# Kernel tuning notes

Hardware: AMD Instinct MI355X
Metric: run time of the kernel (lower is better)

Reference implementation:

```python
import jax, jax.numpy as jnp
from jax import lax
import numpy as np

K = 2000      # self.k: entries kept per sample
T_SC = 3      # number of IHT iterations
DN = ('NCHW', 'OIHW', 'NCHW')


def keep_k_largest(X, k):
    # Per-sample hard threshold: keep the k largest-magnitude entries of the
    # flattened [C,H,W] activations, zero the rest (exactly k kept, as in argsort).
    B = X.shape[0]
    flat = X.reshape(B, -1)                                # [B, N]
    _, idx = lax.top_k(jnp.abs(flat), k)                   # [B, k]
    vals = jnp.take_along_axis(flat, idx, axis=1)          # [B, k]
    out = jnp.zeros_like(flat).at[jnp.arange(B)[:, None], idx].set(vals)
    return out.reshape(X.shape)


def _D_apply(X, W_D):
    # ConvTranspose2d(numb_atom -> dp_channels), stride 1, no padding:
    # full correlation with the spatially flipped, io-swapped kernel.
    kh, kw = W_D.shape[2], W_D.shape[3]
    Wt = jnp.flip(jnp.transpose(W_D, (1, 0, 2, 3)), (2, 3))  # [dp, atoms, kh, kw]
    return lax.conv_general_dilated(X, Wt, (1, 1),
                                    [(kh - 1, kh - 1), (kw - 1, kw - 1)],
                                    dimension_numbers=DN)


def _Dt_apply(Z, W_D):
    # Conv2d(dp_channels -> numb_atom) VALID; D_trans.weight = D.weight.permute(0,1,3,2)
    Wt = jnp.transpose(W_D, (0, 1, 3, 2))                  # [atoms, dp, kh, kw]
    return lax.conv_general_dilated(Z, Wt, (1, 1), 'VALID', dimension_numbers=DN)


def setup_inputs() -> dict:
    key = jax.random.key(0)
    k1, k2, k3 = jax.random.split(key, 3)
    Y = jax.random.normal(k1, (32, 3, 64, 64), jnp.float32)
    X0 = jax.random.normal(k2, (32, 128, 57, 57), jnp.float32)   # random init X in forward
    W_D = jax.random.normal(k3, (128, 3, 8, 8), jnp.float32) * 0.05
    return {"Y": Y, "X0": X0, "W_D": W_D}


def reference(Y, X0, W_D):
    # HT_arg = X - D_trans(D(X) - Y); then T_SC hard-threshold iterations.
    HT_arg = X0 - _Dt_apply(_D_apply(X0, W_D) - Y, W_D)
    X = HT_arg
    for i in range(T_SC):
        X = keep_k_largest(HT_arg, K)
        if i < T_SC - 1:  # final HT_arg update in the original is unused
            HT_arg = X - _Dt_apply(_D_apply(X, W_D) - Y, W_D)
    return X
```

## Files before the change

kernel.cpp:

```cpp
#include <hip/hip_runtime.h>

#define BATCH 32
#define ATOMS 128
#define CCH 3
#define XH 57
#define XW 57
#define OHH 64
#define OWW 64
#define KSEL 2000
#define PIX (XH*XW)
#define NPS (ATOMS*PIX)
#define NTOT (BATCH*NPS)
#define RPS (CCH*OHH*OWW)
#define RTOT (BATCH*RPS)
#define CANDCAP 32768
#define NW 24576
#define WSEG 102

__global__ __launch_bounds__(256) void prep_k(const float* __restrict__ Wg,
    double* __restrict__ WDd, double* __restrict__ Wt2d,
    const float* __restrict__ Y, double* __restrict__ Rd) {
  int e = blockIdx.x * 256 + threadIdx.x;
  if (e < NW) {
    {
      int kw = e & 7; int t = e >> 3; int c = t % 3; t /= 3; int kh = t & 7; int a = t >> 3;
      WDd[e] = (double)Wg[(a*3 + c)*64 + kh*8 + kw];
    }
    {
      int a = e & 127; int t = e >> 7; int j = t & 7; int i = (t >> 3) & 7; int c = t >> 6;
      Wt2d[e] = (double)Wg[(a*3 + c)*64 + j*8 + i];
    }
  }
  if (e < RTOT) Rd[e] = -(double)Y[e];
}

__global__ __launch_bounds__(256) void convD_k(const float* __restrict__ X,
    const double* __restrict__ WDd, double* __restrict__ Rd) {
  __shared__ float Xs[8][11][72];
  int p = blockIdx.x;
  int lg = (p & 7) * 256 + (p >> 3);
  int b = lg >> 6; int rem = lg & 63;
  int band = rem >> 2, quarter = rem & 3;
  int row0 = band * 4;
  int a_base = quarter * 32;
  int tid = threadIdx.x;
  int ox = tid & 63;
  int wv = __builtin_amdgcn_readfirstlane(tid >> 6);
  const float* Xb = X + (size_t)b * NPS;

  double acc[4][3];
#pragma unroll
  for (int ty = 0; ty < 4; ++ty)
#pragma unroll
    for (int c = 0; c < 3; ++c) acc[ty][c] = 0.0;

  for (int ch = 0; ch < 4; ++ch) {
    __syncthreads();
    for (int e = tid; e < 8 * 11 * 72; e += 256) {
      int ai = e / 792; int rem2 = e - ai * 792;
      int r = rem2 / 72; int ss = rem2 - r * 72;
      int gy = row0 - 7 + r;
      int xcol = ss - 7;
      int a = a_base + ch * 8 + ai;
      float v = 0.0f;
      if ((unsigned)xcol < (unsigned)XW && (unsigned)gy < (unsigned)XH)
        v = Xb[a * PIX + gy * XW + xcol];
      Xs[ai][r][ss] = v;
    }
    __syncthreads();
#pragma unroll
    for (int jj = 0; jj < 2; ++jj) {
      int ai = (wv << 1) + jj;
      int a  = a_base + ch * 8 + ai;
      const double* Wa = WDd + a * 192;
#pragma unroll
      for (int r = 0; r < 11; ++r) {
        int gy = row0 - 7 + r;
        if ((unsigned)gy >= (unsigned)XH) continue;
        double xd[8];
#pragma unroll
        for (int t = 0; t < 8; ++t) xd[t] = (double)Xs[ai][r][ox + t];
#pragma unroll
        for (int ty = 0; ty < 4; ++ty) {
          int kh = ty + 7 - r;
          if ((unsigned)kh < 8u) {
            const double* Wk = Wa + kh * 24;
#pragma unroll
            for (int kw = 0; kw < 8; ++kw) {
              acc[ty][0] = fma(xd[7 - kw], Wk[kw],      acc[ty][0]);
              acc[ty][1] = fma(xd[7 - kw], Wk[8 + kw],  acc[ty][1]);
              acc[ty][2] = fma(xd[7 - kw], Wk[16 + kw], acc[ty][2]);
            }
          }
        }
      }
    }
  }
#pragma unroll
  for (int ty = 0; ty < 4; ++ty) {
    int oy = row0 + ty;
#pragma unroll
    for (int c = 0; c < 3; ++c)
      atomicAdd(&Rd[((size_t)(b * CCH + c) << 12) + (oy << 6) + ox], acc[ty][c]);
  }
}

__global__ __launch_bounds__(256) void convD_sparse_k(const float* __restrict__ Wg,
    const int* __restrict__ nzidx, const float* __restrict__ nzval,
    const float* __restrict__ Y, float* __restrict__ R) {
  __shared__ double accd[512];
  __shared__ float Wf[8192];
  __shared__ int   li[KSEL];
  __shared__ float lv[KSEL];
  int p = blockIdx.x;
  int lg = (p & 7) * 96 + (p >> 3);
  int s = lg / 24; int r = lg % 24; int c = r >> 3; int band = r & 7;
  int row0 = band * 8;
  int tid = threadIdx.x;
  for (int e = tid; e < 512; e += 256) accd[e] = 0.0;
  for (int e = tid; e < 8192; e += 256) {
    int a = e >> 6, k2 = e & 63;
    Wf[e] = Wg[(a * 3 + c) * 64 + k2];
  }
  for (int e = tid; e < KSEL; e += 256) {
    li[e] = nzidx[s * KSEL + e];
    lv[e] = nzval[s * KSEL + e];
  }
  __syncthreads();
  int slot = tid >> 3, kw = tid & 7;
  for (int e = slot; e < KSEL; e += 32) {
    int idx = li[e];
    int a = (int)((unsigned)idx / 3249u);
    int pp = idx - a * 3249;
    int y = (int)((unsigned)pp / 57u);
    int x = pp - y * 57;
    int dy = y - row0;
    if (dy < -7 || dy > 7) continue;
    double val = (double)lv[e];
    const float* wp = Wf + (a << 6) + kw;
#pragma unroll
    for (int kh = 0; kh < 8; ++kh) {
      int rr = dy + kh;
      if ((unsigned)rr < 8u)
        __hip_atomic_fetch_add(&accd[(rr << 6) + x + kw],
                               val * (double)wp[kh << 3],
                               __ATOMIC_RELAXED, __HIP_MEMORY_SCOPE_WORKGROUP);
    }
  }
  __syncthreads();
  const float* Yb = Y + (((size_t)(s * CCH + c)) << 12) + (row0 << 6);
  float* Rb = R + (((size_t)(s * CCH + c)) << 12) + (row0 << 6);
  for (int e = tid; e < 512; e += 256)
    Rb[e] = (float)(accd[e] - (double)Yb[e]);
}

template <typename TR>
__global__ __launch_bounds__(256) void convDt_k(const TR* __restrict__ R,
    const double* __restrict__ Wt2d, const float* __restrict__ Xprev,
    float* __restrict__ HT, unsigned* __restrict__ g1) {
  __shared__ float Rl[3][15][72];
  __shared__ unsigned hh[1024];
  int p = blockIdx.x;
  int lg = (p & 7) * 512 + (p >> 3);
  int b = lg >> 7; int rem = lg & 127; int ag = rem >> 3; int by = rem & 7;
  int row0 = by * 8;
  int a0 = ag * 8;
  int tid = threadIdx.x;
  for (int e = tid; e < 1024; e += 256) hh[e] = 0;
  for (int e = tid; e < 3 * 15 * 72; e += 256) {
    int c = e / (15 * 72); int r2 = e - c * (15 * 72);
    int rr = r2 / 72; int cc = r2 - rr * 72;
    int gr = row0 + rr;
    float v = 0.0f;
    if (cc < OWW && gr < OHH)
      v = (float)R[((size_t)(b * CCH + c) << 12) + (gr << 6) + cc];
    Rl[c][rr][cc] = v;
  }
  __syncthreads();
  int x = tid & 63, yg = tid >> 6;
  int yb = yg * 2;
  double acc[8][2];
#pragma unroll
  for (int aa = 0; aa < 8; ++aa) { acc[aa][0] = 0.0; acc[aa][1] = 0.0; }

#pragma unroll 1
  for (int c = 0; c < 3; ++c) {
#pragma unroll 1
    for (int j = 0; j < 8; ++j) {
      double rw[9];
#pragma unroll
      for (int r = 0; r < 9; ++r) rw[r] = (double)Rl[c][yb + r][x + j];
#pragma unroll
      for (int i = 0; i < 8; ++i) {
        const double* wp = Wt2d + ((c * 8 + i) * 8 + j) * 128 + a0;
#pragma unroll
        for (int aa = 0; aa < 8; ++aa) {
          double w = wp[aa];
          acc[aa][0] = fma(rw[i + 0], w, acc[aa][0]);
          acc[aa][1] = fma(rw[i + 1], w, acc[aa][1]);
        }
      }
    }
  }
  if (x < XW) {
#pragma unroll
    for (int ty = 0; ty < 2; ++ty) {
      int yy = row0 + yb + ty;
      if (yy < XH) {
#pragma unroll
        for (int aa = 0; aa < 8; ++aa) {
          size_t xo = (size_t)(b * ATOMS + a0 + aa) * PIX + yy * XW + x;
          float fv = (float)((double)Xprev[xo] - acc[aa][ty]);
          HT[xo] = fv;
          unsigned u = __float_as_uint(fv) & 0x7fffffffu;
          unsigned bin = u >> 20;
          atomicAdd(&hh[bin >> 1], 1u << ((bin & 1) << 4));
        }
      }
    }
  }
  __syncthreads();
  unsigned* gp = g1 + (size_t)b * 2048;
  for (int e = tid; e < 1024; e += 256) {
    unsigned v = hh[e];
    unsigned lo = v & 0xffffu, hi = v >> 16;
    if (lo) atomicAdd(&gp[2 * e], lo);
    if (hi) atomicAdd(&gp[2 * e + 1], hi);
  }
}

template <int NB>
__global__ __launch_bounds__(256) void find_k(const unsigned* __restrict__ gh,
    const int* __restrict__ Kin, int* __restrict__ Bout, int* __restrict__ Kout) {
  int s = blockIdx.x;
  const unsigned* h = gh + s * NB;
  __shared__ unsigned part[256];
  constexpr int C = NB / 256;
  int t = threadIdx.x;
  unsigned sum = 0;
#pragma unroll
  for (int e = 0; e < C; ++e) sum += h[t * C + e];
  part[t] = sum;
  __syncthreads();
  if (t == 0) {
    int Kv = Kin ? Kin[s] : KSEL;
    unsigned cumBefore = 0;
    int bsel = 0;
    for (int q = 255; q >= 0; --q) {
      unsigned ps = part[q];
      if ((int)(cumBefore + ps) >= Kv) {
        for (int e = q * C + C - 1;; --e) {
          unsigned c2 = cumBefore + h[e];
          if ((int)c2 >= Kv) { bsel = e; break; }
          cumBefore = c2;
        }
        break;
      }
      cumBefore += ps;
    }
    Bout[s] = bsel;
    Kout[s] = Kv - (int)cumBefore;
  }
}

__global__ __launch_bounds__(256) void hist2_k(const float* __restrict__ HT,
    const int* __restrict__ b1, unsigned* __restrict__ g2,
    int* __restrict__ cand, int* __restrict__ candcnt) {
  __shared__ unsigned h[1024];
  __shared__ int lidx[4096];
  __shared__ int lcnt, lbase;
  for (int e = threadIdx.x; e < 1024; e += 256) h[e] = 0;
  if (threadIdx.x == 0) lcnt = 0;
  __syncthreads();
  int s = blockIdx.x >> 5;
  int chunk = blockIdx.x & 31;
  unsigned pre = (unsigned)b1[s];
  const uint4* U4 = (const uint4*)(HT + (size_t)s * NPS);
  for (int i4 = chunk * 256 + threadIdx.x; i4 < NPS / 4; i4 += 32 * 256) {
    uint4 v = U4[i4];
    unsigned uu[4] = {v.x, v.y, v.z, v.w};
#pragma unroll
    for (int t = 0; t < 4; ++t) {
      unsigned u = uu[t] & 0x7fffffffu;
      if ((u >> 20) == pre) {
        atomicAdd(&h[(u >> 10) & 1023], 1u);
        int pos = atomicAdd(&lcnt, 1);
        if (pos < 4096) lidx[pos] = i4 * 4 + t;
      }
    }
  }
  __syncthreads();
  if (threadIdx.x == 0) {
    int n = lcnt < 4096 ? lcnt : 4096;
    lbase = atomicAdd(&candcnt[s], n);
  }
  __syncthreads();
  int n = lcnt < 4096 ? lcnt : 4096;
  int base = lbase;
  for (int e = threadIdx.x; e < n; e += 256) {
    int g = base + e;
    if (g < CANDCAP) cand[s * CANDCAP + g] = lidx[e];
  }
  for (int e = threadIdx.x; e < 1024; e += 256)
    if (h[e]) atomicAdd(&g2[s * 1024 + e], h[e]);
}

__global__ __launch_bounds__(256) void pass3_k(const float* __restrict__ HT,
    const int* __restrict__ cand, const int* __restrict__ candcnt,
    const int* __restrict__ b1, const unsigned* __restrict__ g2,
    const int* __restrict__ k1, unsigned* __restrict__ tau_out,
    int* __restrict__ cutoff_out) {
  int s = blockIdx.x;
  __shared__ unsigned h[1024];
  __shared__ unsigned part[256];
  __shared__ int eqidx[1024];
  __shared__ int eqn;
  __shared__ unsigned tau_sh;
  __shared__ int k3_sh;
  __shared__ int b2_sh, k2_sh;
  int t = threadIdx.x;
  const unsigned* hg = g2 + s * 1024;
  unsigned sum = 0;
#pragma unroll
  for (int e = 0; e < 4; ++e) sum += hg[t * 4 + e];
  part[t] = sum;
  for (int e = t; e < 1024; e += 256) h[e] = 0;
  if (t == 0) eqn = 0;
  __syncthreads();
  if (t == 0) {
    int Kv = k1[s];
    unsigned cumBefore = 0;
    int bsel = 0;
    for (int q = 255; q >= 0; --q) {
      unsigned ps = part[q];
      if ((int)(cumBefore + ps) >= Kv) {
        for (int e = q * 4 + 3;; --e) {
          unsigned c2 = cumBefore + hg[e];
          if ((int)c2 >= Kv) { bsel = e; break; }
          cumBefore = c2;
        }
        break;
      }
      cumBefore += ps;
    }
    b2_sh = bsel;
    k2_sh = Kv - (int)cumBefore;
  }
  __syncthreads();
  int n = candcnt[s];
  if (n > CANDCAP) n = CANDCAP;
  unsigned pre21 = (((unsigned)b1[s]) << 10) | (unsigned)b2_sh;
  const unsigned* U = (const unsigned*)(HT + (size_t)s * NPS);
  for (int e = t; e < n; e += 256) {
    int i = cand[s * CANDCAP + e];
    unsigned u = U[i] & 0x7fffffffu;
    if ((u >> 10) == pre21) atomicAdd(&h[u & 1023], 1u);
  }
  __syncthreads();
  if (t == 0) {
    int Kv = k2_sh;
    unsigned cumBefore = 0;
    int b3 = 0;
    for (int e = 1023; e >= 0; --e) {
      unsigned c2 = cumBefore + h[e];
      if ((int)c2 >= Kv) { b3 = e; break; }
      cumBefore = c2;
    }
    tau_sh = (pre21 << 10) | (unsigned)b3;
    k3_sh = Kv - (int)cumBefore;
  }
  __syncthreads();
  unsigned tau = tau_sh;
  for (int e = t; e < n; e += 256) {
    int i = cand[s * CANDCAP + e];
    unsigned u = U[i] & 0x7fffffffu;
    if (u == tau) {
      int pos = atomicAdd(&eqn, 1);
      if (pos < 1024) eqidx[pos] = i;
    }
  }
  __syncthreads();
  if (t == 0) {
    int m = eqn < 1024 ? eqn : 1024;
    int k3 = k3_sh;
    int cutoff;
    if (k3 >= m) {
      cutoff = 0x7fffffff;
    } else {
      int last = -1;
      for (int r = 0; r < k3; ++r) {
        int mn = 0x7fffffff;
        for (int q = 0; q < m; ++q) {
          int v = eqidx[q];
          if (v > last && v < mn) mn = v;
        }
        last = mn;
      }
      cutoff = last;
    }
    tau_out[s] = tau;
    cutoff_out[s] = cutoff;
  }
}

__global__ __launch_bounds__(256) void write_k(const float* __restrict__ HT,
    const unsigned* __restrict__ tau, const int* __restrict__ cutoff,
    float* __restrict__ Xo, int* __restrict__ nzidx, float* __restrict__ nzval,
    int* __restrict__ nzcnt) {
  __shared__ int lidx[2048];
  __shared__ float lval[2048];
  __shared__ int lcnt, lbase;
  int s = blockIdx.x / WSEG;
  int seg = blockIdx.x % WSEG;
  int tid = threadIdx.x;
  bool emit = (nzidx != nullptr);
  if (tid == 0) lcnt = 0;
  __syncthreads();
  unsigned tt = tau[s];
  int co = cutoff[s];
  size_t sbase = (size_t)s * NPS;
  const float4* H4 = (const float4*)(HT + sbase);
  float4* X4 = (float4*)(Xo + sbase);
  int f0 = seg * 1024;
#pragma unroll
  for (int rr = 0; rr < 4; ++rr) {
    int i4 = f0 + rr * 256 + tid;
    if (i4 < NPS / 4) {
      float4 v = H4[i4];
      float vv[4] = {v.x, v.y, v.z, v.w};
      float oo[4];
#pragma unroll
      for (int t = 0; t < 4; ++t) {
        int il = i4 * 4 + t;
        unsigned u = __float_as_uint(vv[t]) & 0x7fffffffu;
        bool keep = (u > tt) || (u == tt && il <= co);
        oo[t] = keep ? vv[t] : 0.0f;
        if (keep && emit) {
          int pos = atomicAdd(&lcnt, 1);
          if (pos < 2048) { lidx[pos] = il; lval[pos] = vv[t]; }
        }
      }
      X4[i4] = make_float4(oo[0], oo[1], oo[2], oo[3]);
    }
  }
  if (!emit) return;
  __syncthreads();
  if (tid == 0) lbase = atomicAdd(&nzcnt[s], lcnt);
  __syncthreads();
  int n = lcnt < 2048 ? lcnt : 2048;
  int base = lbase;
  for (int e = tid; e < n; e += 256) {
    int g = base + e;
    if (g < KSEL) { nzidx[s * KSEL + g] = lidx[e]; nzval[s * KSEL + g] = lval[e]; }
  }
}

extern "C" void kernel_launch(void* const* d_in, const int* in_sizes, int n_in,
                              void* d_out, int out_size, void* d_ws, size_t ws_size,
                              hipStream_t stream) {
  const float* Y  = (const float*)d_in[0];
  const float* X0 = (const float*)d_in[1];
  const float* Wg = (const float*)d_in[2];
  float* Xout = (float*)d_out;

  double* WDd  = (double*)d_ws;
  double* Wt2d = WDd + NW;
  float* HT   = (float*)(Wt2d + NW);
  float* Rbuf = HT + NTOT;
  double* Rd  = (double*)(Rbuf + RTOT);
  unsigned* g1 = (unsigned*)(Rd + RTOT);
  unsigned* g2 = g1 + 32 * 2048;
  int* candcnt = (int*)(g2 + 32 * 1024);
  int* nzcnt = candcnt + 32;
  int* b1 = nzcnt + 32;
  int* k1 = b1 + 32;
  unsigned* tau = (unsigned*)(k1 + 32);
  int* cutoff = (int*)(tau + 32);
  int* cand = cutoff + 32;
  int* nzidx = cand + 32 * CANDCAP;
  float* nzval = (float*)(nzidx + 32 * KSEL);
  size_t zero_bytes = (size_t)(32 * 2048 + 32 * 1024 + 32 + 32) * 4;

  prep_k<<<dim3((RTOT + 255) / 256), dim3(256), 0, stream>>>(Wg, WDd, Wt2d, Y, Rd);

  for (int it = 0; it < 3; ++it) {
    const float* Xsrc = (it == 0) ? X0 : (const float*)Xout;
    hipMemsetAsync(g1, 0, zero_bytes, stream);
    if (it == 0) {
      convD_k<<<dim3(2048), dim3(256), 0, stream>>>(Xsrc, WDd, Rd);
      convDt_k<double><<<dim3(4096), dim3(256), 0, stream>>>(Rd, Wt2d, Xsrc, HT, g1);
    } else {
      convD_sparse_k<<<dim3(BATCH * CCH * 8), dim3(256), 0, stream>>>(
          Wg, nzidx, nzval, Y, Rbuf);
      convDt_k<float><<<dim3(4096), dim3(256), 0, stream>>>(Rbuf, Wt2d, Xsrc, HT, g1);
    }
    find_k<2048><<<dim3(BATCH), dim3(256), 0, stream>>>(g1, (const int*)nullptr, b1, k1);
    hist2_k<<<dim3(BATCH * 32), dim3(256), 0, stream>>>(HT, b1, g2, cand, candcnt);
    pass3_k<<<dim3(BATCH), dim3(256), 0, stream>>>(HT, cand, candcnt, b1, g2, k1, tau, cutoff);
    bool last = (it == 2);
    write_k<<<dim3(BATCH * WSEG), dim3(256), 0, stream>>>(HT, tau, cutoff, Xout,
        last ? nullptr : nzidx, last ? nullptr : nzval, nzcnt);
  }
}
```

Measured before the change: 1.006 ms.

## Rebuild sparse X in shared memory and drop dense X writes until last iteration

In iterations after the first, convDt now scatters the sparse nonzero list (nzidx/nzval) into a shared-memory tile instead of reading the dense previous X from global memory. Because of that, write_k only stores the dense thresholded X on the final iteration. The separate find_k launch is removed, and the first-level histogram bin selection is recomputed redundantly inside hist2_k and pass3_k. Together these cut large dense global reads and writes plus one launch per iteration, at the cost of extra shared memory, a scan over 2000 nonzeros per block, and duplicated prefix-scan work.

```diff
diff --git a/kernel.cpp b/kernel.cpp
--- a/kernel.cpp
+++ b/kernel.cpp
@@ -154,12 +154,14 @@
     Rb[e] = (float)(accd[e] - (double)Yb[e]);
 }
 
-template <typename TR>
+template <typename TR, bool SPX>
 __global__ __launch_bounds__(256) void convDt_k(const TR* __restrict__ R,
     const double* __restrict__ Wt2d, const float* __restrict__ Xprev,
+    const int* __restrict__ nzidx, const float* __restrict__ nzval,
     float* __restrict__ HT, unsigned* __restrict__ g1) {
   __shared__ float Rl[3][15][72];
   __shared__ unsigned hh[1024];
+  __shared__ float Xp[8][8][XW];
   int p = blockIdx.x;
   int lg = (p & 7) * 512 + (p >> 3);
   int b = lg >> 7; int rem = lg & 127; int ag = rem >> 3; int by = rem & 7;
@@ -176,6 +178,19 @@
       v = (float)R[((size_t)(b * CCH + c) << 12) + (gr << 6) + cc];
     Rl[c][rr][cc] = v;
   }
+  if constexpr (SPX) {
+    for (int e = tid; e < 8 * 8 * XW; e += 256) (&Xp[0][0][0])[e] = 0.0f;
+    __syncthreads();
+    for (int e = tid; e < KSEL; e += 256) {
+      int idx = nzidx[b * KSEL + e];
+      int a = (int)((unsigned)idx / 3249u);
+      int pp2 = idx - a * 3249;
+      int yy = (int)((unsigned)pp2 / 57u);
+      int xx = pp2 - yy * 57;
+      if ((unsigned)(a - a0) < 8u && (unsigned)(yy - row0) < 8u)
+        Xp[a - a0][yy - row0][xx] = nzval[b * KSEL + e];
+    }
+  }
   __syncthreads();
   int x = tid & 63, yg = tid >> 6;
   int yb = yg * 2;
@@ -210,7 +225,10 @@
 #pragma unroll
         for (int aa = 0; aa < 8; ++aa) {
           size_t xo = (size_t)(b * ATOMS + a0 + aa) * PIX + yy * XW + x;
-          float fv = (float)((double)Xprev[xo] - acc[aa][ty]);
+          double xprev;
+          if constexpr (SPX) xprev = (double)Xp[aa][yb + ty][x];
+          else               xprev = (double)Xprev[xo];
+          float fv = (float)(xprev - acc[aa][ty]);
           HT[xo] = fv;
           unsigned u = __float_as_uint(fv) & 0x7fffffffu;
           unsigned bin = u >> 20;
@@ -229,28 +247,33 @@
   }
 }
 
-template <int NB>
-__global__ __launch_bounds__(256) void find_k(const unsigned* __restrict__ gh,
-    const int* __restrict__ Kin, int* __restrict__ Bout, int* __restrict__ Kout) {
-  int s = blockIdx.x;
-  const unsigned* h = gh + s * NB;
+__global__ __launch_bounds__(256) void hist2_k(const float* __restrict__ HT,
+    const unsigned* __restrict__ g1, unsigned* __restrict__ g2,
+    int* __restrict__ cand, int* __restrict__ candcnt) {
+  __shared__ unsigned h[1024];
   __shared__ unsigned part[256];
-  constexpr int C = NB / 256;
-  int t = threadIdx.x;
-  unsigned sum = 0;
-#pragma unroll
-  for (int e = 0; e < C; ++e) sum += h[t * C + e];
-  part[t] = sum;
-  __syncthreads();
-  if (t == 0) {
-    int Kv = Kin ? Kin[s] : KSEL;
+  __shared__ int lidx[4096];
+  __shared__ int lcnt, lbase, b1_sh;
+  int tid = threadIdx.x;
+  int s = blockIdx.x >> 5;
+  int chunk = blockIdx.x & 31;
+  const unsigned* hg1 = g1 + (size_t)s * 2048;
+  unsigned psum = 0;
+#pragma unroll
+  for (int e = 0; e < 8; ++e) psum += hg1[tid * 8 + e];
+  part[tid] = psum;
+  for (int e = tid; e < 1024; e += 256) h[e] = 0;
+  if (tid == 0) lcnt = 0;
+  __syncthreads();
+  if (tid == 0) {
+    int Kv = KSEL;
     unsigned cumBefore = 0;
     int bsel = 0;
     for (int q = 255; q >= 0; --q) {
       unsigned ps = part[q];
       if ((int)(cumBefore + ps) >= Kv) {
-        for (int e = q * C + C - 1;; --e) {
-          unsigned c2 = cumBefore + h[e];
+        for (int e = q * 8 + 7;; --e) {
+          unsigned c2 = cumBefore + hg1[e];
           if ((int)c2 >= Kv) { bsel = e; break; }
           cumBefore = c2;
         }
@@ -258,25 +281,12 @@
       }
       cumBefore += ps;
     }
-    Bout[s] = bsel;
-    Kout[s] = Kv - (int)cumBefore;
-  }
-}
-
-__global__ __launch_bounds__(256) void hist2_k(const float* __restrict__ HT,
-    const int* __restrict__ b1, unsigned* __restrict__ g2,
-    int* __restrict__ cand, int* __restrict__ candcnt) {
-  __shared__ unsigned h[1024];
-  __shared__ int lidx[4096];
-  __shared__ int lcnt, lbase;
-  for (int e = threadIdx.x; e < 1024; e += 256) h[e] = 0;
-  if (threadIdx.x == 0) lcnt = 0;
-  __syncthreads();
-  int s = blockIdx.x >> 5;
-  int chunk = blockIdx.x & 31;
-  unsigned pre = (unsigned)b1[s];
+    b1_sh = bsel;
+  }
+  __syncthreads();
+  unsigned pre = (unsigned)b1_sh;
   const uint4* U4 = (const uint4*)(HT + (size_t)s * NPS);
-  for (int i4 = chunk * 256 + threadIdx.x; i4 < NPS / 4; i4 += 32 * 256) {
+  for (int i4 = chunk * 256 + tid; i4 < NPS / 4; i4 += 32 * 256) {
     uint4 v = U4[i4];
     unsigned uu[4] = {v.x, v.y, v.z, v.w};
 #pragma unroll
@@ -290,26 +300,25 @@
     }
   }
   __syncthreads();
-  if (threadIdx.x == 0) {
+  if (tid == 0) {
     int n = lcnt < 4096 ? lcnt : 4096;
     lbase = atomicAdd(&candcnt[s], n);
   }
   __syncthreads();
   int n = lcnt < 4096 ? lcnt : 4096;
   int base = lbase;
-  for (int e = threadIdx.x; e < n; e += 256) {
+  for (int e = tid; e < n; e += 256) {
     int g = base + e;
     if (g < CANDCAP) cand[s * CANDCAP + g] = lidx[e];
   }
-  for (int e = threadIdx.x; e < 1024; e += 256)
+  for (int e = tid; e < 1024; e += 256)
     if (h[e]) atomicAdd(&g2[s * 1024 + e], h[e]);
 }
 
 __global__ __launch_bounds__(256) void pass3_k(const float* __restrict__ HT,
     const int* __restrict__ cand, const int* __restrict__ candcnt,
-    const int* __restrict__ b1, const unsigned* __restrict__ g2,
-    const int* __restrict__ k1, unsigned* __restrict__ tau_out,
-    int* __restrict__ cutoff_out) {
+    const unsigned* __restrict__ g1, const unsigned* __restrict__ g2,
+    unsigned* __restrict__ tau_out, int* __restrict__ cutoff_out) {
   int s = blockIdx.x;
   __shared__ unsigned h[1024];
   __shared__ unsigned part[256];
@@ -317,18 +326,44 @@
   __shared__ int eqn;
   __shared__ unsigned tau_sh;
   __shared__ int k3_sh;
-  __shared__ int b2_sh, k2_sh;
+  __shared__ int b1_sh, k1_sh, b2_sh, k2_sh;
   int t = threadIdx.x;
-  const unsigned* hg = g2 + s * 1024;
-  unsigned sum = 0;
-#pragma unroll
-  for (int e = 0; e < 4; ++e) sum += hg[t * 4 + e];
-  part[t] = sum;
+  const unsigned* hg1 = g1 + (size_t)s * 2048;
+  unsigned s1 = 0;
+#pragma unroll
+  for (int e = 0; e < 8; ++e) s1 += hg1[t * 8 + e];
+  part[t] = s1;
   for (int e = t; e < 1024; e += 256) h[e] = 0;
   if (t == 0) eqn = 0;
   __syncthreads();
   if (t == 0) {
-    int Kv = k1[s];
+    int Kv = KSEL;
+    unsigned cumBefore = 0;
+    int bsel = 0;
+    for (int q = 255; q >= 0; --q) {
+      unsigned ps = part[q];
+      if ((int)(cumBefore + ps) >= Kv) {
+        for (int e = q * 8 + 7;; --e) {
+          unsigned c2 = cumBefore + hg1[e];
+          if ((int)c2 >= Kv) { bsel = e; break; }
+          cumBefore = c2;
+        }
+        break;
+      }
+      cumBefore += ps;
+    }
+    b1_sh = bsel;
+    k1_sh = Kv - (int)cumBefore;
+  }
+  __syncthreads();
+  const unsigned* hg = g2 + s * 1024;
+  unsigned s2 = 0;
+#pragma unroll
+  for (int e = 0; e < 4; ++e) s2 += hg[t * 4 + e];
+  part[t] = s2;
+  __syncthreads();
+  if (t == 0) {
+    int Kv = k1_sh;
     unsigned cumBefore = 0;
     int bsel = 0;
     for (int q = 255; q >= 0; --q) {
@@ -349,7 +384,7 @@
   __syncthreads();
   int n = candcnt[s];
   if (n > CANDCAP) n = CANDCAP;
-  unsigned pre21 = (((unsigned)b1[s]) << 10) | (unsigned)b2_sh;
+  unsigned pre21 = (((unsigned)b1_sh) << 10) | (unsigned)b2_sh;
   const unsigned* U = (const unsigned*)(HT + (size_t)s * NPS);
   for (int e = t; e < n; e += 256) {
     int i = cand[s * CANDCAP + e];
@@ -406,7 +441,7 @@
 __global__ __launch_bounds__(256) void write_k(const float* __restrict__ HT,
     const unsigned* __restrict__ tau, const int* __restrict__ cutoff,
     float* __restrict__ Xo, int* __restrict__ nzidx, float* __restrict__ nzval,
-    int* __restrict__ nzcnt) {
+    int* __restrict__ nzcnt, int store_x) {
   __shared__ int lidx[2048];
   __shared__ float lval[2048];
   __shared__ int lcnt, lbase;
@@ -440,7 +475,7 @@
           if (pos < 2048) { lidx[pos] = il; lval[pos] = vv[t]; }
         }
       }
-      X4[i4] = make_float4(oo[0], oo[1], oo[2], oo[3]);
+      if (store_x) X4[i4] = make_float4(oo[0], oo[1], oo[2], oo[3]);
     }
   }
   if (!emit) return;
@@ -472,9 +507,7 @@
   unsigned* g2 = g1 + 32 * 2048;
   int* candcnt = (int*)(g2 + 32 * 1024);
   int* nzcnt = candcnt + 32;
-  int* b1 = nzcnt + 32;
-  int* k1 = b1 + 32;
-  unsigned* tau = (unsigned*)(k1 + 32);
+  unsigned* tau = (unsigned*)(nzcnt + 32);
   int* cutoff = (int*)(tau + 32);
   int* cand = cutoff + 32;
   int* nzidx = cand + 32 * CANDCAP;
@@ -484,21 +517,21 @@
   prep_k<<<dim3((RTOT + 255) / 256), dim3(256), 0, stream>>>(Wg, WDd, Wt2d, Y, Rd);
 
   for (int it = 0; it < 3; ++it) {
-    const float* Xsrc = (it == 0) ? X0 : (const float*)Xout;
     hipMemsetAsync(g1, 0, zero_bytes, stream);
     if (it == 0) {
-      convD_k<<<dim3(2048), dim3(256), 0, stream>>>(Xsrc, WDd, Rd);
-      convDt_k<double><<<dim3(4096), dim3(256), 0, stream>>>(Rd, Wt2d, Xsrc, HT, g1);
+      convD_k<<<dim3(2048), dim3(256), 0, stream>>>(X0, WDd, Rd);
+      convDt_k<double, false><<<dim3(4096), dim3(256), 0, stream>>>(
+          Rd, Wt2d, X0, nullptr, nullptr, HT, g1);
     } else {
       convD_sparse_k<<<dim3(BATCH * CCH * 8), dim3(256), 0, stream>>>(
           Wg, nzidx, nzval, Y, Rbuf);
-      convDt_k<float><<<dim3(4096), dim3(256), 0, stream>>>(Rbuf, Wt2d, Xsrc, HT, g1);
-    }
-    find_k<2048><<<dim3(BATCH), dim3(256), 0, stream>>>(g1, (const int*)nullptr, b1, k1);
-    hist2_k<<<dim3(BATCH * 32), dim3(256), 0, stream>>>(HT, b1, g2, cand, candcnt);
-    pass3_k<<<dim3(BATCH), dim3(256), 0, stream>>>(HT, cand, candcnt, b1, g2, k1, tau, cutoff);
+      convDt_k<float, true><<<dim3(4096), dim3(256), 0, stream>>>(
+          Rbuf, Wt2d, nullptr, nzidx, nzval, HT, g1);
+    }
+    hist2_k<<<dim3(BATCH * 32), dim3(256), 0, stream>>>(HT, g1, g2, cand, candcnt);
+    pass3_k<<<dim3(BATCH), dim3(256), 0, stream>>>(HT, cand, candcnt, g1, g2, tau, cutoff);
     bool last = (it == 2);
     write_k<<<dim3(BATCH * WSEG), dim3(256), 0, stream>>>(HT, tau, cutoff, Xout,
-        last ? nullptr : nzidx, last ? nullptr : nzval, nzcnt);
-  }
-}
+        last ? nullptr : nzidx, last ? nullptr : nzval, nzcnt, last ? 1 : 0);
+  }
+}
```

Measured after the change: 1.031 ms. +2.5%, slower.
